# Performance work log

Hardware: AMD Instinct MI355X
Metric: run time of the kernel (lower is better)

## Reference

```python
import jax, jax.numpy as jnp
import numpy as np
from jax import lax

SIGMA = 1
KSIZE = SIGMA * 4 + 1  # 5-tap, odd -> torch 'same' == lax 'SAME'


def _gauss1d():
    half = (KSIZE - 1) * 0.5
    x = np.linspace(-half, half, KSIZE)
    pdf = np.exp(-0.5 * (x / SIGMA) ** 2)
    return jnp.asarray(pdf / pdf.sum(), dtype=jnp.float32)


def _blur(x):
    # separable depthwise 3D gaussian blur: three sequential 1D convs (D, H, W)
    k = _gauss1d().astype(x.dtype)
    C = x.shape[1]
    dn = lax.conv_dimension_numbers(x.shape, (C, 1, KSIZE, 1, 1), ('NCDHW', 'OIDHW', 'NCDHW'))
    for ax in range(3):
        kshape = [1, 1, 1]
        kshape[ax] = KSIZE
        w = jnp.broadcast_to(k.reshape(kshape)[None, None], (C, 1, *kshape))
        x = lax.conv_general_dilated(x, w, (1, 1, 1), 'SAME',
                                     dimension_numbers=dn, feature_group_count=C)
    return x


def setup_inputs() -> dict:
    key = jax.random.key(0)
    kA, kB, kM = jax.random.split(key, 3)
    shape = (2, 1, 160, 192, 224)
    return {
        'image_A': jax.random.normal(kA, shape, dtype=jnp.float32),
        'image_B': jax.random.normal(kB, shape, dtype=jnp.float32),
        'mask_A': jax.random.uniform(kM, shape, dtype=jnp.float32),
    }


def reference(image_A, image_B, mask_A):
    I, J = image_A, image_B
    bI = _blur(I)
    bJ = _blur(J)
    cross = _blur(I * J) - bI * bJ
    varI = jax.nn.relu(_blur(I * I) - bI ** 2) + 1e-05
    varJ = jax.nn.relu(_blur(J * J) - bJ ** 2) + 1e-05
    lncc = 1.0 - cross / jnp.sqrt(varI * varJ)
    return jnp.sum(lncc * mask_A) / (jnp.sum(mask_A) + 1e-08)
```

## Files before the change

kernel.cpp:

```cpp
#include <hip/hip_runtime.h>


#define NB 2
#define DD 160
#define HH 192
#define WW 224
#define SH 224
#define SD (224*192)
#define SN (224*192*160)

#define TW 32
#define TH 16
#define ROWS (TH+4)
#define DCHUNK 20
#define NCHUNK (DD/DCHUNK)

#define K0 0.05448868f
#define K1 0.24420134f
#define K2 0.40261995f

typedef float v2f __attribute__((ext_vector_type(2)));
typedef float v4f __attribute__((ext_vector_type(4)));

__global__ __launch_bounds__(640) void lncc_main(
    const float* __restrict__ A, const float* __restrict__ B,
    const float* __restrict__ M, double* __restrict__ acc)
{
    __shared__ v2f  sIJ[2][ROWS][36];
    __shared__ v4f  wbA[2][ROWS][32];
    __shared__ float wbC[2][ROWS][32];
    __shared__ float redL[10], redM[10];

    const int wt = blockIdx.x;
    const int ht = blockIdx.y;
    const int zz = blockIdx.z;
    const int n  = zz >> 3;
    const int dc = zz & 7;
    const int w0 = wt * TW, h0 = ht * TH, d0 = dc * DCHUNK;

    const float* __restrict__ Ai = A + (size_t)n * SN;
    const float* __restrict__ Bi = B + (size_t)n * SN;
    const float* __restrict__ Mi = M + (size_t)n * SN;

    const int tid = threadIdx.x;
    const int r   = tid >> 5;
    const int c   = tid & 31;

    const int gh  = h0 + r - 2;
    const bool hv = (unsigned)gh < (unsigned)HH;
    const int ghc = hv ? gh : 0;
    const int hwm = ghc * SH + (w0 + c);
    const int gwl = w0 + c - 2, gwr = w0 + c + 2;
    const bool lv = hv && (c < 2)   && (gwl >= 0);
    const bool rv = hv && (c >= 30) && (gwr < WW);
    const bool anyh = lv || rv;
    const int hwh = ghc * SH + (lv ? gwl : (rv ? gwr : 0));
    const int mbase = (h0 + r) * SH + (w0 + c);

    v2f pP0 = 0.f, pP1 = 0.f, pP2 = 0.f, pP3 = 0.f;
    v2f pQ0 = 0.f, pQ1 = 0.f, pQ2 = 0.f, pQ3 = 0.f;
    float pC0 = 0.f, pC1 = 0.f, pC2 = 0.f, pC3 = 0.f;
    float accL = 0.f, accM = 0.f;

    v2f nM = 0.f, nH = 0.f;
    {
        const int dd = d0 - 2;
        if (dd >= 0) {
            const int dof = dd * SD;
            if (hv)   { nM.x = Ai[dof + hwm]; nM.y = Bi[dof + hwm]; }
            if (anyh) { nH.x = Ai[dof + hwh]; nH.y = Bi[dof + hwh]; }
        }
    }

    const int NIT = DCHUNK + 6;
#pragma unroll 2
    for (int k = 0; k < NIT; ++k) {
        const int pw = k & 1;
        const int px = pw ^ 1;

        if (k < DCHUNK + 4) {
            sIJ[pw][r][c + 2] = nM;
            if (c < 2)        sIJ[pw][r][c]     = nH;
            else if (c >= 30) sIJ[pw][r][c + 4] = nH;
        }

        nM = 0.f; nH = 0.f;
        {
            const int dd = d0 - 1 + k;
            if ((k + 1 < DCHUNK + 4) && (dd >= 0) && (dd < DD)) {
                const int dof = dd * SD;
                if (hv)   { nM.x = Ai[dof + hwm]; nM.y = Bi[dof + hwm]; }
                if (anyh) { nH.x = Ai[dof + hwh]; nH.y = Bi[dof + hwh]; }
            }
        }
        const int  dout = d0 - 6 + k;
        const bool outv = (k >= 6) && (r < TH);
        float mval = 0.f;
        if (outv) mval = Mi[dout * SD + mbase];

        if (k >= 1 && k <= DCHUNK + 4) {
            const v2f v0 = sIJ[px][r][c];
            const v2f v1 = sIJ[px][r][c + 1];
            const v2f v2 = sIJ[px][r][c + 2];
            const v2f v3 = sIJ[px][r][c + 3];
            const v2f v4 = sIJ[px][r][c + 4];
            const v2f b  = K0*(v0+v4) + K1*(v1+v3) + K2*v2;
            const v2f bs = K0*(v0*v0+v4*v4) + K1*(v1*v1+v3*v3) + K2*(v2*v2);
            const float bij = K0*(v0.x*v0.y+v4.x*v4.y) + K1*(v1.x*v1.y+v3.x*v3.y) + K2*(v2.x*v2.y);
            wbA[px][r][c] = (v4f){b.x, b.y, bs.x, bs.y};
            wbC[px][r][c] = bij;
        }

        if (k >= 2 && r < TH) {
            const v4f a0 = wbA[pw][r][c];
            const v4f a1 = wbA[pw][r + 1][c];
            const v4f a2 = wbA[pw][r + 2][c];
            const v4f a3 = wbA[pw][r + 3][c];
            const v4f a4 = wbA[pw][r + 4][c];
            const float c0 = wbC[pw][r][c];
            const float c1 = wbC[pw][r + 1][c];
            const float c2 = wbC[pw][r + 2][c];
            const float c3 = wbC[pw][r + 3][c];
            const float c4 = wbC[pw][r + 4][c];
            const v2f h1 = K0*(a0.xy+a4.xy) + K1*(a1.xy+a3.xy) + K2*a2.xy;
            const v2f h2 = K0*(a0.zw+a4.zw) + K1*(a1.zw+a3.zw) + K2*a2.zw;
            const float hc = K0*(c0+c4) + K1*(c1+c3) + K2*c2;

            if (outv) {
                const v2f bP = K0*(pP0+h1) + K1*(pP1+pP3) + K2*pP2;
                const v2f bS = K0*(pQ0+h2) + K1*(pQ1+pQ3) + K2*pQ2;
                const float bC = K0*(pC0+hc) + K1*(pC1+pC3) + K2*pC2;
                const float cross = bC - bP.x * bP.y;
                const float vI = fmaxf(bS.x - bP.x * bP.x, 0.f) + 1e-5f;
                const float vJ = fmaxf(bS.y - bP.y * bP.y, 0.f) + 1e-5f;
                const float lncc = 1.0f - cross * rsqrtf(vI * vJ);
                accL += lncc * mval;
                accM += mval;
            }

            pP0 = pP1; pP1 = pP2; pP2 = pP3; pP3 = h1;
            pQ0 = pQ1; pQ1 = pQ2; pQ2 = pQ3; pQ3 = h2;
            pC0 = pC1; pC1 = pC2; pC2 = pC3; pC3 = hc;
        }

        asm volatile("s_waitcnt lgkmcnt(0)\n\ts_barrier" ::: "memory");
    }

#pragma unroll
    for (int off = 32; off > 0; off >>= 1) {
        accL += __shfl_down(accL, off, 64);
        accM += __shfl_down(accM, off, 64);
    }
    const int wave = tid >> 6;
    if ((tid & 63) == 0) { redL[wave] = accL; redM[wave] = accM; }
    __syncthreads();
    if (tid == 0) {
        float sL = 0.f, sM = 0.f;
#pragma unroll
        for (int kk = 0; kk < 10; ++kk) { sL += redL[kk]; sM += redM[kk]; }
        atomicAdd(&acc[0], (double)sL);
        atomicAdd(&acc[1], (double)sM);
    }
}

__global__ void lncc_final(const double* __restrict__ acc, float* __restrict__ out)
{
    out[0] = (float)(acc[0] / (acc[1] + 1e-8));
}

extern "C" void kernel_launch(void* const* d_in, const int* in_sizes, int n_in,
                              void* d_out, int out_size, void* d_ws, size_t ws_size,
                              hipStream_t stream)
{
    const float* A = (const float*)d_in[0];
    const float* B = (const float*)d_in[1];
    const float* M = (const float*)d_in[2];
    double* acc = (double*)d_ws;

    hipMemsetAsync(d_ws, 0, 2 * sizeof(double), stream);

    dim3 grid(WW / TW, HH / TH, NB * NCHUNK);
    dim3 block(640);
    hipLaunchKernelGGL(lncc_main, grid, block, 0, stream, A, B, M, acc);
    hipLaunchKernelGGL(lncc_final, dim3(1), dim3(1), 0, stream, acc, (float*)d_out);
}
```

Before: 228.8 us.

## Compute two H-rows per thread with taller tile and shorter depth chunk

Each thread now handles two adjacent rows of the H dimension, so the tile height doubles to 32 while the depth chunk halves to 10. The vertical blur pass shares six LDS reads across both outputs instead of five per output, which cuts LDS traffic and lowers the H-halo overhead per output. In exchange the depth-halo overhead per chunk grows (4 extra planes per 10 instead of per 20), the register state per thread roughly doubles, and some threads in the 640-thread block sit idle during the staging and output stages.

```diff
diff --git a/kernel.cpp b/kernel.cpp
--- a/kernel.cpp
+++ b/kernel.cpp
@@ -10,9 +10,9 @@
 #define SN (224*192*160)
 
 #define TW 32
-#define TH 16
+#define TH 32
 #define ROWS (TH+4)
-#define DCHUNK 20
+#define DCHUNK 10
 #define NCHUNK (DD/DCHUNK)
 
 #define K0 0.05448868f
@@ -34,8 +34,8 @@
     const int wt = blockIdx.x;
     const int ht = blockIdx.y;
     const int zz = blockIdx.z;
-    const int n  = zz >> 3;
-    const int dc = zz & 7;
+    const int n  = zz >> 4;
+    const int dc = zz & 15;
     const int w0 = wt * TW, h0 = ht * TH, d0 = dc * DCHUNK;
 
     const float* __restrict__ Ai = A + (size_t)n * SN;
@@ -43,32 +43,52 @@
     const float* __restrict__ Mi = M + (size_t)n * SN;
 
     const int tid = threadIdx.x;
-    const int r   = tid >> 5;
+    const int rr  = tid >> 5;
     const int c   = tid & 31;
-
-    const int gh  = h0 + r - 2;
-    const bool hv = (unsigned)gh < (unsigned)HH;
-    const int ghc = hv ? gh : 0;
-    const int hwm = ghc * SH + (w0 + c);
+    const int sa  = rr * 2;
+    const int sb  = sa + 1;
+    const bool stv = (rr < 18);
+    const bool orv = (rr < 16);
+
+    const int gha = h0 + sa - 2;
+    const int ghb = gha + 1;
+    const bool hva = stv && ((unsigned)gha < (unsigned)HH);
+    const bool hvb = stv && ((unsigned)ghb < (unsigned)HH);
+    const int ghca = hva ? gha : 0;
+    const int ghcb = hvb ? ghb : 0;
+    const int hwma = ghca * SH + (w0 + c);
+    const int hwmb = ghcb * SH + (w0 + c);
+
     const int gwl = w0 + c - 2, gwr = w0 + c + 2;
-    const bool lv = hv && (c < 2)   && (gwl >= 0);
-    const bool rv = hv && (c >= 30) && (gwr < WW);
-    const bool anyh = lv || rv;
-    const int hwh = ghc * SH + (lv ? gwl : (rv ? gwr : 0));
-    const int mbase = (h0 + r) * SH + (w0 + c);
-
-    v2f pP0 = 0.f, pP1 = 0.f, pP2 = 0.f, pP3 = 0.f;
-    v2f pQ0 = 0.f, pQ1 = 0.f, pQ2 = 0.f, pQ3 = 0.f;
-    float pC0 = 0.f, pC1 = 0.f, pC2 = 0.f, pC3 = 0.f;
+    const bool lc = (c < 2)   && (gwl >= 0);
+    const bool rc = (c >= 30) && (gwr < WW);
+    const int  whx = lc ? gwl : (rc ? gwr : 0);
+    const bool anyc  = lc || rc;
+    const bool anyha = anyc && hva;
+    const bool anyhb = anyc && hvb;
+    const int hwha = ghca * SH + whx;
+    const int hwhb = ghcb * SH + whx;
+
+    const int mbasea = (h0 + sa) * SH + (w0 + c);
+    const int mbaseb = mbasea + SH;
+
+    v2f pP0a=0.f,pP1a=0.f,pP2a=0.f,pP3a=0.f;
+    v2f pQ0a=0.f,pQ1a=0.f,pQ2a=0.f,pQ3a=0.f;
+    float pC0a=0.f,pC1a=0.f,pC2a=0.f,pC3a=0.f;
+    v2f pP0b=0.f,pP1b=0.f,pP2b=0.f,pP3b=0.f;
+    v2f pQ0b=0.f,pQ1b=0.f,pQ2b=0.f,pQ3b=0.f;
+    float pC0b=0.f,pC1b=0.f,pC2b=0.f,pC3b=0.f;
     float accL = 0.f, accM = 0.f;
 
-    v2f nM = 0.f, nH = 0.f;
+    v2f nMa = 0.f, nMb = 0.f, nHa = 0.f, nHb = 0.f;
     {
         const int dd = d0 - 2;
         if (dd >= 0) {
             const int dof = dd * SD;
-            if (hv)   { nM.x = Ai[dof + hwm]; nM.y = Bi[dof + hwm]; }
-            if (anyh) { nH.x = Ai[dof + hwh]; nH.y = Bi[dof + hwh]; }
+            if (hva)  { nMa.x = Ai[dof + hwma]; nMa.y = Bi[dof + hwma]; }
+            if (hvb)  { nMb.x = Ai[dof + hwmb]; nMb.y = Bi[dof + hwmb]; }
+            if (anyha){ nHa.x = Ai[dof + hwha]; nHa.y = Bi[dof + hwha]; }
+            if (anyhb){ nHb.x = Ai[dof + hwhb]; nHb.y = Bi[dof + hwhb]; }
         }
     }
 
@@ -78,69 +98,118 @@
         const int pw = k & 1;
         const int px = pw ^ 1;
 
-        if (k < DCHUNK + 4) {
-            sIJ[pw][r][c + 2] = nM;
-            if (c < 2)        sIJ[pw][r][c]     = nH;
-            else if (c >= 30) sIJ[pw][r][c + 4] = nH;
-        }
-
-        nM = 0.f; nH = 0.f;
+        if (k < DCHUNK + 4 && stv) {
+            sIJ[pw][sa][c + 2] = nMa;
+            sIJ[pw][sb][c + 2] = nMb;
+            if (c < 2) {
+                sIJ[pw][sa][c] = nHa;
+                sIJ[pw][sb][c] = nHb;
+            } else if (c >= 30) {
+                sIJ[pw][sa][c + 4] = nHa;
+                sIJ[pw][sb][c + 4] = nHb;
+            }
+        }
+
+        nMa = 0.f; nMb = 0.f; nHa = 0.f; nHb = 0.f;
         {
             const int dd = d0 - 1 + k;
             if ((k + 1 < DCHUNK + 4) && (dd >= 0) && (dd < DD)) {
                 const int dof = dd * SD;
-                if (hv)   { nM.x = Ai[dof + hwm]; nM.y = Bi[dof + hwm]; }
-                if (anyh) { nH.x = Ai[dof + hwh]; nH.y = Bi[dof + hwh]; }
-            }
-        }
+                if (hva)  { nMa.x = Ai[dof + hwma]; nMa.y = Bi[dof + hwma]; }
+                if (hvb)  { nMb.x = Ai[dof + hwmb]; nMb.y = Bi[dof + hwmb]; }
+                if (anyha){ nHa.x = Ai[dof + hwha]; nHa.y = Bi[dof + hwha]; }
+                if (anyhb){ nHb.x = Ai[dof + hwhb]; nHb.y = Bi[dof + hwhb]; }
+            }
+        }
+
         const int  dout = d0 - 6 + k;
-        const bool outv = (k >= 6) && (r < TH);
-        float mval = 0.f;
-        if (outv) mval = Mi[dout * SD + mbase];
-
-        if (k >= 1 && k <= DCHUNK + 4) {
-            const v2f v0 = sIJ[px][r][c];
-            const v2f v1 = sIJ[px][r][c + 1];
-            const v2f v2 = sIJ[px][r][c + 2];
-            const v2f v3 = sIJ[px][r][c + 3];
-            const v2f v4 = sIJ[px][r][c + 4];
-            const v2f b  = K0*(v0+v4) + K1*(v1+v3) + K2*v2;
-            const v2f bs = K0*(v0*v0+v4*v4) + K1*(v1*v1+v3*v3) + K2*(v2*v2);
-            const float bij = K0*(v0.x*v0.y+v4.x*v4.y) + K1*(v1.x*v1.y+v3.x*v3.y) + K2*(v2.x*v2.y);
-            wbA[px][r][c] = (v4f){b.x, b.y, bs.x, bs.y};
-            wbC[px][r][c] = bij;
-        }
-
-        if (k >= 2 && r < TH) {
-            const v4f a0 = wbA[pw][r][c];
-            const v4f a1 = wbA[pw][r + 1][c];
-            const v4f a2 = wbA[pw][r + 2][c];
-            const v4f a3 = wbA[pw][r + 3][c];
-            const v4f a4 = wbA[pw][r + 4][c];
-            const float c0 = wbC[pw][r][c];
-            const float c1 = wbC[pw][r + 1][c];
-            const float c2 = wbC[pw][r + 2][c];
-            const float c3 = wbC[pw][r + 3][c];
-            const float c4 = wbC[pw][r + 4][c];
-            const v2f h1 = K0*(a0.xy+a4.xy) + K1*(a1.xy+a3.xy) + K2*a2.xy;
-            const v2f h2 = K0*(a0.zw+a4.zw) + K1*(a1.zw+a3.zw) + K2*a2.zw;
-            const float hc = K0*(c0+c4) + K1*(c1+c3) + K2*c2;
+        const bool outv = (k >= 6) && orv;
+        float mvala = 0.f, mvalb = 0.f;
+        if (outv) {
+            mvala = Mi[dout * SD + mbasea];
+            mvalb = Mi[dout * SD + mbaseb];
+        }
+
+        if (k >= 1 && k <= DCHUNK + 4 && stv) {
+            {
+                const v2f v0 = sIJ[px][sa][c];
+                const v2f v1 = sIJ[px][sa][c + 1];
+                const v2f v2 = sIJ[px][sa][c + 2];
+                const v2f v3 = sIJ[px][sa][c + 3];
+                const v2f v4 = sIJ[px][sa][c + 4];
+                const v2f b  = K0*(v0+v4) + K1*(v1+v3) + K2*v2;
+                const v2f bs = K0*(v0*v0+v4*v4) + K1*(v1*v1+v3*v3) + K2*(v2*v2);
+                const float bij = K0*(v0.x*v0.y+v4.x*v4.y) + K1*(v1.x*v1.y+v3.x*v3.y) + K2*(v2.x*v2.y);
+                wbA[px][sa][c] = (v4f){b.x, b.y, bs.x, bs.y};
+                wbC[px][sa][c] = bij;
+            }
+            {
+                const v2f v0 = sIJ[px][sb][c];
+                const v2f v1 = sIJ[px][sb][c + 1];
+                const v2f v2 = sIJ[px][sb][c + 2];
+                const v2f v3 = sIJ[px][sb][c + 3];
+                const v2f v4 = sIJ[px][sb][c + 4];
+                const v2f b  = K0*(v0+v4) + K1*(v1+v3) + K2*v2;
+                const v2f bs = K0*(v0*v0+v4*v4) + K1*(v1*v1+v3*v3) + K2*(v2*v2);
+                const float bij = K0*(v0.x*v0.y+v4.x*v4.y) + K1*(v1.x*v1.y+v3.x*v3.y) + K2*(v2.x*v2.y);
+                wbA[px][sb][c] = (v4f){b.x, b.y, bs.x, bs.y};
+                wbC[px][sb][c] = bij;
+            }
+        }
+
+        if (k >= 2 && orv) {
+            const v4f a0 = wbA[pw][sa    ][c];
+            const v4f a1 = wbA[pw][sa + 1][c];
+            const v4f a2 = wbA[pw][sa + 2][c];
+            const v4f a3 = wbA[pw][sa + 3][c];
+            const v4f a4 = wbA[pw][sa + 4][c];
+            const v4f a5 = wbA[pw][sa + 5][c];
+            const float e0 = wbC[pw][sa    ][c];
+            const float e1 = wbC[pw][sa + 1][c];
+            const float e2 = wbC[pw][sa + 2][c];
+            const float e3 = wbC[pw][sa + 3][c];
+            const float e4 = wbC[pw][sa + 4][c];
+            const float e5 = wbC[pw][sa + 5][c];
+
+            const v2f h1a = K0*(a0.xy+a4.xy) + K1*(a1.xy+a3.xy) + K2*a2.xy;
+            const v2f h2a = K0*(a0.zw+a4.zw) + K1*(a1.zw+a3.zw) + K2*a2.zw;
+            const float hca = K0*(e0+e4) + K1*(e1+e3) + K2*e2;
+
+            const v2f h1b = K0*(a1.xy+a5.xy) + K1*(a2.xy+a4.xy) + K2*a3.xy;
+            const v2f h2b = K0*(a1.zw+a5.zw) + K1*(a2.zw+a4.zw) + K2*a3.zw;
+            const float hcb = K0*(e1+e5) + K1*(e2+e4) + K2*e3;
 
             if (outv) {
-                const v2f bP = K0*(pP0+h1) + K1*(pP1+pP3) + K2*pP2;
-                const v2f bS = K0*(pQ0+h2) + K1*(pQ1+pQ3) + K2*pQ2;
-                const float bC = K0*(pC0+hc) + K1*(pC1+pC3) + K2*pC2;
-                const float cross = bC - bP.x * bP.y;
-                const float vI = fmaxf(bS.x - bP.x * bP.x, 0.f) + 1e-5f;
-                const float vJ = fmaxf(bS.y - bP.y * bP.y, 0.f) + 1e-5f;
-                const float lncc = 1.0f - cross * rsqrtf(vI * vJ);
-                accL += lncc * mval;
-                accM += mval;
-            }
-
-            pP0 = pP1; pP1 = pP2; pP2 = pP3; pP3 = h1;
-            pQ0 = pQ1; pQ1 = pQ2; pQ2 = pQ3; pQ3 = h2;
-            pC0 = pC1; pC1 = pC2; pC2 = pC3; pC3 = hc;
+                {
+                    const v2f bP = K0*(pP0a+h1a) + K1*(pP1a+pP3a) + K2*pP2a;
+                    const v2f bS = K0*(pQ0a+h2a) + K1*(pQ1a+pQ3a) + K2*pQ2a;
+                    const float bC = K0*(pC0a+hca) + K1*(pC1a+pC3a) + K2*pC2a;
+                    const float cross = bC - bP.x * bP.y;
+                    const float vI = fmaxf(bS.x - bP.x * bP.x, 0.f) + 1e-5f;
+                    const float vJ = fmaxf(bS.y - bP.y * bP.y, 0.f) + 1e-5f;
+                    const float lncc = 1.0f - cross * rsqrtf(vI * vJ);
+                    accL += lncc * mvala;
+                    accM += mvala;
+                }
+                {
+                    const v2f bP = K0*(pP0b+h1b) + K1*(pP1b+pP3b) + K2*pP2b;
+                    const v2f bS = K0*(pQ0b+h2b) + K1*(pQ1b+pQ3b) + K2*pQ2b;
+                    const float bC = K0*(pC0b+hcb) + K1*(pC1b+pC3b) + K2*pC2b;
+                    const float cross = bC - bP.x * bP.y;
+                    const float vI = fmaxf(bS.x - bP.x * bP.x, 0.f) + 1e-5f;
+                    const float vJ = fmaxf(bS.y - bP.y * bP.y, 0.f) + 1e-5f;
+                    const float lncc = 1.0f - cross * rsqrtf(vI * vJ);
+                    accL += lncc * mvalb;
+                    accM += mvalb;
+                }
+            }
+
+            pP0a=pP1a; pP1a=pP2a; pP2a=pP3a; pP3a=h1a;
+            pQ0a=pQ1a; pQ1a=pQ2a; pQ2a=pQ3a; pQ3a=h2a;
+            pC0a=pC1a; pC1a=pC2a; pC2a=pC3a; pC3a=hca;
+            pP0b=pP1b; pP1b=pP2b; pP2b=pP3b; pP3b=h1b;
+            pQ0b=pQ1b; pQ1b=pQ2b; pQ2b=pQ3b; pQ3b=h2b;
+            pC0b=pC1b; pC1b=pC2b; pC2b=pC3b; pC3b=hcb;
         }
 
         asm volatile("s_waitcnt lgkmcnt(0)\n\ts_barrier" ::: "memory");
```

Result: slower. 237.7 us (+3.9%).
